# Kernel optimization log

Hardware: AMD Instinct MI355X
Metric: run time of the kernel (lower is better)

Reference implementation:

```python
import jax, jax.numpy as jnp
import numpy as np

B, N, CIN, H, E = 1, 20000, 128, 128, 320000


def setup_inputs() -> dict:
    key = jax.random.key(0)
    ks = jax.random.split(key, 16)
    x = jax.random.normal(ks[0], (B, N, CIN), jnp.float32)
    edge_index = jax.random.randint(ks[1], (2, E), 0, N, dtype=jnp.int64)
    edge_weight = jax.random.uniform(ks[2], (E,), jnp.float32)
    h = jax.random.normal(ks[3], (B, N, H), jnp.float32)
    c = jax.random.normal(ks[4], (B, N, H), jnp.float32)
    # GCN stack params, gate order [i, f, c, o]; 2 layers each (K=2)
    Wx0 = jax.random.normal(ks[5], (4, CIN, H), jnp.float32) / np.float32(np.sqrt(CIN))
    bx0 = jnp.zeros((4, H), jnp.float32)
    Wx1 = jax.random.normal(ks[6], (4, H, H), jnp.float32) / np.float32(np.sqrt(H))
    bx1 = jnp.zeros((4, H), jnp.float32)
    Wh0 = jax.random.normal(ks[7], (4, H, H), jnp.float32) / np.float32(np.sqrt(H))
    bh0 = jnp.zeros((4, H), jnp.float32)
    Wh1 = jax.random.normal(ks[8], (4, H, H), jnp.float32) / np.float32(np.sqrt(H))
    bh1 = jnp.zeros((4, H), jnp.float32)
    wc = jax.random.normal(ks[9], (3, H), jnp.float32) * 0.1  # peephole [i, f, o]
    bg = jnp.zeros((4, H), jnp.float32)  # gate biases [i, f, c, o]
    return dict(x=x, edge_index=edge_index, edge_weight=edge_weight, h=h, c=c,
                Wx0=Wx0, bx0=bx0, Wx1=Wx1, bx1=bx1,
                Wh0=Wh0, bh0=bh0, Wh1=Wh1, bh1=bh1, wc=wc, bg=bg)


def reference(x, edge_index, edge_weight, h, c,
              Wx0, bx0, Wx1, bx1, Wh0, bh0, Wh1, bh1, wc, bg):
    n = x.shape[1]
    src, dst = edge_index[0], edge_index[1]
    loop = jnp.arange(n)
    src2 = jnp.concatenate([src, loop])
    dst2 = jnp.concatenate([dst, loop])
    w2 = jnp.concatenate([edge_weight, jnp.ones((n,), edge_weight.dtype)])
    deg = jax.ops.segment_sum(w2, dst2, num_segments=n)
    dis = jnp.where(deg > 0, jax.lax.rsqrt(jnp.maximum(deg, 1e-12)), 0.0)
    norm = dis[src2] * w2 * dis[dst2]  # sym GCN norm with self loops

    def prop(t):  # t: [..., N, F] -> D^-1/2 (A+I) D^-1/2 t
        lead = t.shape[:-2]
        tf = t.reshape((-1,) + t.shape[-2:])
        m = tf[:, src2, :] * norm[None, :, None]
        agg = jax.vmap(lambda mm: jax.ops.segment_sum(mm, dst2, num_segments=n))(m)
        return agg.reshape(lead + agg.shape[-2:])

    def gcn4(t, W0, b0, W1, b1):  # 2-layer GCN, 4 gates at once
        a = prop(t)  # shared first aggregation: [B,N,F]
        h0 = jax.nn.relu(jnp.einsum('bnc,gch->gbnh', a, W0) + b0[:, None, None, :])
        a1 = prop(h0)  # [4,B,N,H]
        return jnp.einsum('gbnh,ghk->gbnk', a1, W1) + b1[:, None, None, :]

    G = gcn4(x, Wx0, bx0, Wx1, bx1) + gcn4(h, Wh0, bh0, Wh1, bh1)  # [4,B,N,H]
    I = jax.nn.sigmoid(G[0] + wc[0] * c + bg[0])
    F = jax.nn.sigmoid(G[1] + wc[1] * c + bg[1])
    T = jnp.tanh(G[2] + bg[2])
    Cn = F * c + I * T
    O = jax.nn.sigmoid(G[3] + wc[2] * Cn + bg[3])
    Hn = O * jnp.tanh(Cn)
    return (Hn, Cn)
```

## Files before the change

kernel.cpp:

```cpp
#include <hip/hip_runtime.h>
#include <hip/hip_bf16.h>
#include <stdint.h>

#define NN    20000
#define NP    20096
#define EE    320000
#define CH    128
#define GC    512
#define NHtot 2560000

typedef short bf16x8 __attribute__((ext_vector_type(8)));
typedef float f32x4  __attribute__((ext_vector_type(4)));

__device__ __forceinline__ unsigned short f2bf(float f) {
    __hip_bfloat16 b = __float2bfloat16(f);
    union { __hip_bfloat16 b; unsigned short u; } c; c.b = b; return c.u;
}
__device__ __forceinline__ void fma4(uint2 u, float n, float* acc) {
    union { unsigned int i; float f; } t;
    t.i = u.x << 16;         acc[0] += n * t.f;
    t.i = u.x & 0xffff0000u; acc[1] += n * t.f;
    t.i = u.y << 16;         acc[2] += n * t.f;
    t.i = u.y & 0xffff0000u; acc[3] += n * t.f;
}
__device__ __forceinline__ void tof4(uint2 u, float* f) {
    union { unsigned int i; float f; } t;
    t.i = u.x << 16;         f[0] = t.f;
    t.i = u.x & 0xffff0000u; f[1] = t.f;
    t.i = u.y << 16;         f[2] = t.f;
    t.i = u.y & 0xffff0000u; f[3] = t.f;
}
__device__ __forceinline__ uint2 pack4(const float* f) {
    uint2 v;
    v.x = (unsigned int)f2bf(f[0]) | ((unsigned int)f2bf(f[1]) << 16);
    v.y = (unsigned int)f2bf(f[2]) | ((unsigned int)f2bf(f[3]) << 16);
    return v;
}

__global__ void k_cntprep(const int* __restrict__ ei, int* __restrict__ cnt,
                          const float* __restrict__ W0, const float* __restrict__ W1,
                          const float* __restrict__ W2, const float* __restrict__ W3,
                          unsigned short* __restrict__ T0, unsigned short* __restrict__ T1,
                          unsigned short* __restrict__ T2, unsigned short* __restrict__ T3,
                          const float* __restrict__ bx1, const float* __restrict__ bh1,
                          const float* __restrict__ bg, float* __restrict__ btot) {
    int bid = blockIdx.x;
    if (bid < EE / 256) {
        int e = bid * 256 + threadIdx.x;
        atomicAdd(&cnt[ei[EE + e]], 1);
        return;
    }
    int pid = bid - EE / 256;
    int z = pid >> 8, y = (pid >> 6) & 3, xb = pid & 63;
    if (z == 0 && y == 0 && xb < 2) {
        int f = xb * 256 + threadIdx.x;
        btot[f] = bx1[f] + bh1[f] + bg[f];
    }
    const float* W; unsigned short* T;
    switch (z) {
        case 0:  W = W0; T = T0; break;
        case 1:  W = W1; T = T1; break;
        case 2:  W = W2; T = T2; break;
        default: W = W3; T = T3; break;
    }
    int n = xb * 2 + (threadIdx.x >> 7);
    int k = threadIdx.x & 127;
    T[((size_t)y * 128 + n) * 128 + k] = f2bf(W[((size_t)y * 128 + k) * 128 + n]);
}

__global__ void k_scan1(const int* __restrict__ cnt, int* __restrict__ rowoff,
                        int* __restrict__ bsum) {
    __shared__ int wsum[4];
    int i = blockIdx.x * 256 + threadIdx.x;
    int self = (i < NN) ? cnt[i] : 0;
    int lane = threadIdx.x & 63, wid = threadIdx.x >> 6;
    int v = self;
    #pragma unroll
    for (int off = 1; off < 64; off <<= 1) {
        int u = __shfl_up(v, off);
        if (lane >= off) v += u;
    }
    if (lane == 63) wsum[wid] = v;
    __syncthreads();
    int wof = 0;
    for (int k = 0; k < wid; ++k) wof += wsum[k];
    if (i < NN) rowoff[i] = wof + v - self;
    if (threadIdx.x == 255) bsum[blockIdx.x] = wof + v;
}

__global__ void k_scan2(int* __restrict__ bsum) {
    int lane = threadIdx.x;
    int base = 0;
    for (int start = 0; start < 80; start += 64) {
        int i = start + lane;
        int self = (i < 80) ? bsum[i] : 0;
        int v = self;
        #pragma unroll
        for (int off = 1; off < 64; off <<= 1) {
            int u = __shfl_up(v, off);
            if (lane >= off) v += u;
        }
        if (i < 80) bsum[i] = base + v - self;
        base += __shfl(v, 63);
    }
}

__global__ void k_scan3(int* __restrict__ rowoff, const int* __restrict__ bsum,
                        int* __restrict__ cur) {
    int i = blockIdx.x * 256 + threadIdx.x;
    if (i < NN) {
        int v = rowoff[i] + bsum[i >> 8];
        rowoff[i] = v; cur[i] = v;
    }
    if (i == NN) rowoff[NN] = EE;
}

__global__ void k_scatter(const int* __restrict__ ei, const float* __restrict__ ew,
                          int* __restrict__ cur,
                          int* __restrict__ csrs, float* __restrict__ csrw) {
    int e = blockIdx.x * 256 + threadIdx.x;
    if (e >= EE) return;
    int s = ei[e], d = ei[EE + e];
    int p = atomicAdd(&cur[d], 1);
    csrs[p] = s; csrw[p] = ew[e];
}

__global__ __launch_bounds__(256) void k_degcast(
        const float* __restrict__ x, const float* __restrict__ h,
        const int* __restrict__ rowoff, const float* __restrict__ csrw,
        float* __restrict__ dis, unsigned short* __restrict__ xhb) {
    int wid = threadIdx.x >> 6, lane = threadIdx.x & 63;
    int w = blockIdx.x * 4 + wid;
    int e0 = rowoff[w], e1 = rowoff[w + 1];
    float s = 0.f;
    for (int e = e0 + lane; e < e1; e += 64) s += csrw[e];
    #pragma unroll
    for (int off = 32; off; off >>= 1) s += __shfl_xor(s, off);
    float dn = rsqrtf(fmaxf(1.0f + s, 1e-12f));
    if (lane == 0) dis[w] = dn;
    const float* src = (lane < 32) ? x + (size_t)w * CH + lane * 4
                                   : h + (size_t)w * CH + (lane - 32) * 4;
    float4 v = *(const float4*)src;
    float f[4] = { dn * v.x, dn * v.y, dn * v.z, dn * v.w };
    *(uint2*)(xhb + (size_t)w * 256 + lane * 4) = pack4(f);
}

__global__ __launch_bounds__(128) void k_prop256(
        const unsigned short* __restrict__ tab, unsigned short* __restrict__ o,
        const int* __restrict__ rowoff, const int* __restrict__ csrs,
        const float* __restrict__ csrw, const float* __restrict__ dis) {
    int w = blockIdx.x * 2 + (threadIdx.x >> 6);
    int lane = threadIdx.x & 63;
    const uint2* T2 = (const uint2*)tab;
    float acc[4];
    tof4(T2[(size_t)w * 64 + lane], acc);
    int e = rowoff[w], e1 = rowoff[w + 1];
    for (; e + 4 <= e1; e += 4) {
        int   s0 = csrs[e],   s1 = csrs[e+1], s2 = csrs[e+2], s3 = csrs[e+3];
        float n0 = csrw[e],   n1 = csrw[e+1], n2 = csrw[e+2], n3 = csrw[e+3];
        uint2 u0 = T2[(size_t)s0 * 64 + lane];
        uint2 u1 = T2[(size_t)s1 * 64 + lane];
        uint2 u2 = T2[(size_t)s2 * 64 + lane];
        uint2 u3 = T2[(size_t)s3 * 64 + lane];
        fma4(u0, n0, acc); fma4(u1, n1, acc); fma4(u2, n2, acc); fma4(u3, n3, acc);
    }
    for (; e < e1; ++e) {
        fma4(T2[(size_t)csrs[e] * 64 + lane], csrw[e], acc);
    }
    float dw = dis[w];
    #pragma unroll
    for (int j = 0; j < 4; ++j) acc[j] *= dw;
    ((uint2*)o)[(size_t)w * 64 + lane] = pack4(acc);
}

#define SWZ(r, c8) (((r) << 4) + ((c8) ^ ((r) & 15)))

__global__ __launch_bounds__(256) void k_gemm1(
        const unsigned short* __restrict__ A,
        const unsigned short* __restrict__ Wtx, const unsigned short* __restrict__ Wth,
        const float* __restrict__ bx0, const float* __restrict__ bh0,
        unsigned short* __restrict__ outx, unsigned short* __restrict__ outh) {
    __shared__ uint4 As[2048];
    __shared__ uint4 Bs[2048];
    const int side = blockIdx.z;
    const int aoff = side * 128;
    const unsigned short* Wt = side ? Wth : Wtx;
    const float* bias        = side ? bh0 : bx0;
    unsigned short* out      = side ? outh : outx;

    const int    g    = blockIdx.y;
    const size_t row0 = (size_t)blockIdx.x * 128;
    const int    t    = threadIdx.x;

    #pragma unroll
    for (int p = 0; p < 8; ++p) {
        int id = t + 256 * p, r = id >> 4, c8 = id & 15;
        As[SWZ(r, c8)] = *(const uint4*)(A + (row0 + r) * 256 + aoff + c8 * 8);
    }
    const unsigned short* Wg = Wt + (size_t)g * 16384;
    #pragma unroll
    for (int p = 0; p < 8; ++p) {
        int id = t + 256 * p, r = id >> 4, c8 = id & 15;
        Bs[SWZ(r, c8)] = *(const uint4*)(Wg + r * CH + c8 * 8);
    }
    __syncthreads();

    const int wid = t >> 6, l = t & 63;
    const int m0 = (wid >> 1) * 64, n0 = (wid & 1) * 64;
    const int lm = l & 15, q = l >> 4;
    f32x4 acc[4][4];
    #pragma unroll
    for (int i = 0; i < 4; ++i)
        #pragma unroll
        for (int j = 0; j < 4; ++j) { acc[i][j][0]=0.f; acc[i][j][1]=0.f; acc[i][j][2]=0.f; acc[i][j][3]=0.f; }

    #pragma unroll
    for (int kc = 0; kc < 4; ++kc) {
        int c8 = kc * 4 + q;
        bf16x8 a[4], b[4];
        #pragma unroll
        for (int i = 0; i < 4; ++i) { int r = m0 + i * 16 + lm; a[i] = *(const bf16x8*)&As[SWZ(r, c8)]; }
        #pragma unroll
        for (int j = 0; j < 4; ++j) { int r = n0 + j * 16 + lm; b[j] = *(const bf16x8*)&Bs[SWZ(r, c8)]; }
        #pragma unroll
        for (int i = 0; i < 4; ++i)
            #pragma unroll
            for (int j = 0; j < 4; ++j)
                acc[i][j] = __builtin_amdgcn_mfma_f32_16x16x32_bf16(a[i], b[j], acc[i][j], 0, 0, 0);
    }

    #pragma unroll
    for (int j = 0; j < 4; ++j) {
        float bb = bias[g * CH + n0 + j * 16 + lm];
        #pragma unroll
        for (int i = 0; i < 4; ++i)
            #pragma unroll
            for (int r = 0; r < 4; ++r) {
                int rowl = m0 + i * 16 + q * 4 + r;
                int col  = n0 + j * 16 + lm;
                out[(row0 + rowl) * GC + g * CH + col] = f2bf(fmaxf(acc[i][j][r] + bb, 0.f));
            }
    }
}

__global__ __launch_bounds__(256) void k_gemm2(
        const unsigned short* __restrict__ A1, const unsigned short* __restrict__ A2,
        const unsigned short* __restrict__ Wt1, const unsigned short* __restrict__ Wt2,
        const float* __restrict__ dis, unsigned short* __restrict__ outS) {
    __shared__ uint4 As[2048];
    __shared__ uint4 Bs[2048];
    const int    g    = blockIdx.y;
    const size_t row0 = (size_t)blockIdx.x * 128;
    const int    t    = threadIdx.x;
    const int wid = t >> 6, l = t & 63;
    const int m0 = (wid >> 1) * 64, n0 = (wid & 1) * 64;
    const int lm = l & 15, q = l >> 4;
    f32x4 acc[4][4];
    #pragma unroll
    for (int i = 0; i < 4; ++i)
        #pragma unroll
        for (int j = 0; j < 4; ++j) { acc[i][j][0]=0.f; acc[i][j][1]=0.f; acc[i][j][2]=0.f; acc[i][j][3]=0.f; }

    for (int side = 0; side < 2; ++side) {
        if (side) __syncthreads();
        const unsigned short* Ap = side ? A2 : A1;
        const unsigned short* Wg = (side ? Wt2 : Wt1) + (size_t)g * 16384;
        #pragma unroll
        for (int p = 0; p < 8; ++p) {
            int id = t + 256 * p, r = id >> 4, c8 = id & 15;
            As[SWZ(r, c8)] = *(const uint4*)(Ap + (row0 + r) * GC + g * CH + c8 * 8);
        }
        #pragma unroll
        for (int p = 0; p < 8; ++p) {
            int id = t + 256 * p, r = id >> 4, c8 = id & 15;
            Bs[SWZ(r, c8)] = *(const uint4*)(Wg + r * CH + c8 * 8);
        }
        __syncthreads();
        #pragma unroll
        for (int kc = 0; kc < 4; ++kc) {
            int c8 = kc * 4 + q;
            bf16x8 a[4], b[4];
            #pragma unroll
            for (int i = 0; i < 4; ++i) { int r = m0 + i * 16 + lm; a[i] = *(const bf16x8*)&As[SWZ(r, c8)]; }
            #pragma unroll
            for (int j = 0; j < 4; ++j) { int r = n0 + j * 16 + lm; b[j] = *(const bf16x8*)&Bs[SWZ(r, c8)]; }
            #pragma unroll
            for (int i = 0; i < 4; ++i)
                #pragma unroll
                for (int j = 0; j < 4; ++j)
                    acc[i][j] = __builtin_amdgcn_mfma_f32_16x16x32_bf16(a[i], b[j], acc[i][j], 0, 0, 0);
        }
    }

    #pragma unroll
    for (int j = 0; j < 4; ++j)
        #pragma unroll
        for (int i = 0; i < 4; ++i)
            #pragma unroll
            for (int r = 0; r < 4; ++r) {
                int rowl = m0 + i * 16 + q * 4 + r;
                int col  = n0 + j * 16 + lm;
                float dr = dis[row0 + rowl];
                outS[(row0 + rowl) * GC + g * CH + col] = f2bf(dr * acc[i][j][r]);
            }
}

#define GIDX(f) ((f) + ((f) >> 5))
__global__ __launch_bounds__(128) void k_prop512g(
        const unsigned short* __restrict__ Sb, float* __restrict__ out,
        const int* __restrict__ rowoff, const int* __restrict__ csrs,
        const float* __restrict__ csrw, const float* __restrict__ dis,
        const float* __restrict__ c, const float* __restrict__ btot,
        const float* __restrict__ wc) {
    __shared__ float gbuf[528];
    int half = threadIdx.x >> 6, lane = threadIdx.x & 63;
    int w = blockIdx.x;
    const uint2* S2 = (const uint2*)Sb;
    size_t foff = (size_t)half * 64 + lane;
    float acc[4];
    tof4(S2[(size_t)w * 128 + foff], acc);
    int e = rowoff[w], e1 = rowoff[w + 1];
    for (; e + 4 <= e1; e += 4) {
        int   s0 = csrs[e],   s1 = csrs[e+1], s2 = csrs[e+2], s3 = csrs[e+3];
        float n0 = csrw[e],   n1 = csrw[e+1], n2 = csrw[e+2], n3 = csrw[e+3];
        uint2 u0 = S2[(size_t)s0 * 128 + foff];
        uint2 u1 = S2[(size_t)s1 * 128 + foff];
        uint2 u2 = S2[(size_t)s2 * 128 + foff];
        uint2 u3 = S2[(size_t)s3 * 128 + foff];
        fma4(u0, n0, acc); fma4(u1, n1, acc); fma4(u2, n2, acc); fma4(u3, n3, acc);
    }
    for (; e < e1; ++e) {
        fma4(S2[(size_t)csrs[e] * 128 + foff], csrw[e], acc);
    }
    float dw = dis[w];
    #pragma unroll
    for (int j = 0; j < 4; ++j) {
        int f = half * 256 + lane * 4 + j;
        gbuf[GIDX(f)] = dw * acc[j];
    }
    __syncthreads();
    int hh = threadIdx.x;
    float g0 = gbuf[GIDX(hh)]       + btot[hh];
    float g1 = gbuf[GIDX(128 + hh)] + btot[128 + hh];
    float g2 = gbuf[GIDX(256 + hh)] + btot[256 + hh];
    float g3 = gbuf[GIDX(384 + hh)] + btot[384 + hh];
    float cv = c[(size_t)w * CH + hh];
    float I  = 1.f / (1.f + expf(-(g0 + wc[hh]       * cv)));
    float F  = 1.f / (1.f + expf(-(g1 + wc[128 + hh] * cv)));
    float T  = tanhf(g2);
    float Cn = F * cv + I * T;
    float O  = 1.f / (1.f + expf(-(g3 + wc[256 + hh] * Cn)));
    out[(size_t)w * CH + hh]         = O * tanhf(Cn);
    out[NHtot + (size_t)w * CH + hh] = Cn;
}

extern "C" void kernel_launch(void* const* d_in, const int* in_sizes, int n_in,
                              void* d_out, int out_size, void* d_ws, size_t ws_size,
                              hipStream_t stream) {
    (void)in_sizes; (void)n_in; (void)out_size; (void)ws_size;
    const float* x   = (const float*)d_in[0];
    const int*   ei  = (const int*)d_in[1];
    const float* ew  = (const float*)d_in[2];
    const float* h   = (const float*)d_in[3];
    const float* c   = (const float*)d_in[4];
    const float* Wx0 = (const float*)d_in[5];
    const float* bx0 = (const float*)d_in[6];
    const float* Wx1 = (const float*)d_in[7];
    const float* bx1 = (const float*)d_in[8];
    const float* Wh0 = (const float*)d_in[9];
    const float* bh0 = (const float*)d_in[10];
    const float* Wh1 = (const float*)d_in[11];
    const float* bh1 = (const float*)d_in[12];
    const float* wc  = (const float*)d_in[13];
    const float* bg  = (const float*)d_in[14];
    float* out = (float*)d_out;

    float* wsf  = (float*)d_ws;
    float* dis  = wsf;
    int*   cnt  = (int*)(wsf + 20480);
    int*   row  = (int*)(wsf + 40960);
    int*   cur  = (int*)(wsf + 61696);
    int*   bsum = (int*)(wsf + 82176);
    float* btot = wsf + 82432;
    int*   csrs = (int*)(wsf + 82944);
    float* csrw = wsf + 402944;
    unsigned short* Wt0x = (unsigned short*)(wsf + 722944);
    unsigned short* Wt0h = (unsigned short*)(wsf + 755712);
    unsigned short* Wt1x = (unsigned short*)(wsf + 788480);
    unsigned short* Wt1h = (unsigned short*)(wsf + 821248);
    unsigned short* xhb  = (unsigned short*)(wsf + 854016);
    unsigned short* axh  = (unsigned short*)(wsf + 3426304);
    unsigned short* h0x  = (unsigned short*)(wsf + 5998592);
    unsigned short* h0h  = (unsigned short*)(wsf + 11143168);
    unsigned short* Sb   = (unsigned short*)(wsf + 16287744);

    hipMemsetAsync(cnt, 0, 20480 * sizeof(int), stream);

    k_cntprep<<<EE / 256 + 1024, 256, 0, stream>>>(ei, cnt,
                                                   Wx0, Wh0, Wx1, Wh1,
                                                   Wt0x, Wt0h, Wt1x, Wt1h,
                                                   bx1, bh1, bg, btot);
    k_scan1  <<<80, 256, 0, stream>>>(cnt, row, bsum);
    k_scan2  <<<1, 64, 0, stream>>>(bsum);
    k_scan3  <<<80, 256, 0, stream>>>(row, bsum, cur);
    k_scatter<<<EE / 256, 256, 0, stream>>>(ei, ew, cur, csrs, csrw);

    k_degcast<<<NN / 4, 256, 0, stream>>>(x, h, row, csrw, dis, xhb);

    k_prop256<<<NN / 2, 128, 0, stream>>>(xhb, axh, row, csrs, csrw, dis);

    dim3 g1(NP / 128, 4, 2);
    k_gemm1<<<g1, 256, 0, stream>>>(axh, Wt0x, Wt0h, bx0, bh0, h0x, h0h);
    dim3 g2(NP / 128, 4);
    k_gemm2<<<g2, 256, 0, stream>>>(h0x, h0h, Wt1x, Wt1h, dis, Sb);

    k_prop512g<<<NN, 128, 0, stream>>>(Sb, out, row, csrs, csrw, dis, c, btot, wc);
}
```

Baseline: 258.1 us.

## Merge scan passes, fuse degree into count atomics, and unroll gather loops

Edge degree sums are now accumulated with float atomics during the count pass instead of a per-node CSR reduction. The three-kernel scan is replaced by a single 1024-thread block scan, and the scatter and degree/cast kernels are merged into one launch. This cuts several launches and serial dependencies. The propagation gather loops gain an 8-wide unrolled body to put more loads in flight. The cost is extra float atomics and nondeterministic degree summation order.

```diff
diff --git a/kernel.cpp b/kernel.cpp
--- a/kernel.cpp
+++ b/kernel.cpp
@@ -37,7 +37,8 @@
     return v;
 }
 
-__global__ void k_cntprep(const int* __restrict__ ei, int* __restrict__ cnt,
+__global__ void k_cntprep(const int* __restrict__ ei, const float* __restrict__ ew,
+                          int* __restrict__ cnt, float* __restrict__ deg,
                           const float* __restrict__ W0, const float* __restrict__ W1,
                           const float* __restrict__ W2, const float* __restrict__ W3,
                           unsigned short* __restrict__ T0, unsigned short* __restrict__ T1,
@@ -47,7 +48,9 @@
     int bid = blockIdx.x;
     if (bid < EE / 256) {
         int e = bid * 256 + threadIdx.x;
-        atomicAdd(&cnt[ei[EE + e]], 1);
+        int d = ei[EE + e];
+        atomicAdd(&cnt[d], 1);
+        atomicAdd(&deg[d], ew[e]);
         return;
     }
     int pid = bid - EE / 256;
@@ -68,75 +71,57 @@
     T[((size_t)y * 128 + n) * 128 + k] = f2bf(W[((size_t)y * 128 + k) * 128 + n]);
 }
 
-__global__ void k_scan1(const int* __restrict__ cnt, int* __restrict__ rowoff,
-                        int* __restrict__ bsum) {
-    __shared__ int wsum[4];
-    int i = blockIdx.x * 256 + threadIdx.x;
-    int self = (i < NN) ? cnt[i] : 0;
-    int lane = threadIdx.x & 63, wid = threadIdx.x >> 6;
-    int v = self;
+__global__ __launch_bounds__(1024) void k_scanA(const int* __restrict__ cnt,
+                                                int* __restrict__ rowoff,
+                                                int* __restrict__ cur) {
+    __shared__ int wtot[16];
+    int t = threadIdx.x;
+    int base = t * 20;
+    int loc[20];
+    int s = 0;
+    #pragma unroll
+    for (int j = 0; j < 20; ++j) {
+        int i = base + j;
+        int v = (i < NN) ? cnt[i] : 0;
+        loc[j] = s; s += v;
+    }
+    int lane = t & 63, wv = t >> 6;
+    int ps = s;
     #pragma unroll
     for (int off = 1; off < 64; off <<= 1) {
-        int u = __shfl_up(v, off);
-        if (lane >= off) v += u;
-    }
-    if (lane == 63) wsum[wid] = v;
+        int u = __shfl_up(ps, off);
+        if (lane >= off) ps += u;
+    }
+    if (lane == 63) wtot[wv] = ps;
     __syncthreads();
     int wof = 0;
-    for (int k = 0; k < wid; ++k) wof += wsum[k];
-    if (i < NN) rowoff[i] = wof + v - self;
-    if (threadIdx.x == 255) bsum[blockIdx.x] = wof + v;
-}
-
-__global__ void k_scan2(int* __restrict__ bsum) {
-    int lane = threadIdx.x;
-    int base = 0;
-    for (int start = 0; start < 80; start += 64) {
-        int i = start + lane;
-        int self = (i < 80) ? bsum[i] : 0;
-        int v = self;
-        #pragma unroll
-        for (int off = 1; off < 64; off <<= 1) {
-            int u = __shfl_up(v, off);
-            if (lane >= off) v += u;
-        }
-        if (i < 80) bsum[i] = base + v - self;
-        base += __shfl(v, 63);
-    }
-}
-
-__global__ void k_scan3(int* __restrict__ rowoff, const int* __restrict__ bsum,
-                        int* __restrict__ cur) {
-    int i = blockIdx.x * 256 + threadIdx.x;
-    if (i < NN) {
-        int v = rowoff[i] + bsum[i >> 8];
-        rowoff[i] = v; cur[i] = v;
-    }
-    if (i == NN) rowoff[NN] = EE;
-}
-
-__global__ void k_scatter(const int* __restrict__ ei, const float* __restrict__ ew,
+    for (int k = 0; k < wv; ++k) wof += wtot[k];
+    int tstart = wof + ps - s;
+    #pragma unroll
+    for (int j = 0; j < 20; ++j) {
+        int i = base + j;
+        if (i < NN) { int v = tstart + loc[j]; rowoff[i] = v; cur[i] = v; }
+    }
+    if (t == 0) rowoff[NN] = EE;
+}
+
+__global__ void k_scatdeg(const int* __restrict__ ei, const float* __restrict__ ew,
                           int* __restrict__ cur,
-                          int* __restrict__ csrs, float* __restrict__ csrw) {
-    int e = blockIdx.x * 256 + threadIdx.x;
-    if (e >= EE) return;
-    int s = ei[e], d = ei[EE + e];
-    int p = atomicAdd(&cur[d], 1);
-    csrs[p] = s; csrw[p] = ew[e];
-}
-
-__global__ __launch_bounds__(256) void k_degcast(
-        const float* __restrict__ x, const float* __restrict__ h,
-        const int* __restrict__ rowoff, const float* __restrict__ csrw,
-        float* __restrict__ dis, unsigned short* __restrict__ xhb) {
+                          int* __restrict__ csrs, float* __restrict__ csrw,
+                          const float* __restrict__ deg,
+                          const float* __restrict__ x, const float* __restrict__ h,
+                          float* __restrict__ dis, unsigned short* __restrict__ xhb) {
+    int bid = blockIdx.x;
+    if (bid < EE / 256) {
+        int e = bid * 256 + threadIdx.x;
+        int s = ei[e], d = ei[EE + e];
+        int p = atomicAdd(&cur[d], 1);
+        csrs[p] = s; csrw[p] = ew[e];
+        return;
+    }
     int wid = threadIdx.x >> 6, lane = threadIdx.x & 63;
-    int w = blockIdx.x * 4 + wid;
-    int e0 = rowoff[w], e1 = rowoff[w + 1];
-    float s = 0.f;
-    for (int e = e0 + lane; e < e1; e += 64) s += csrw[e];
-    #pragma unroll
-    for (int off = 32; off; off >>= 1) s += __shfl_xor(s, off);
-    float dn = rsqrtf(fmaxf(1.0f + s, 1e-12f));
+    int w = (bid - EE / 256) * 4 + wid;
+    float dn = rsqrtf(fmaxf(1.0f + deg[w], 1e-12f));
     if (lane == 0) dis[w] = dn;
     const float* src = (lane < 32) ? x + (size_t)w * CH + lane * 4
                                    : h + (size_t)w * CH + (lane - 32) * 4;
@@ -155,6 +140,22 @@
     float acc[4];
     tof4(T2[(size_t)w * 64 + lane], acc);
     int e = rowoff[w], e1 = rowoff[w + 1];
+    for (; e + 8 <= e1; e += 8) {
+        int   s0 = csrs[e],   s1 = csrs[e+1], s2 = csrs[e+2], s3 = csrs[e+3];
+        int   s4 = csrs[e+4], s5 = csrs[e+5], s6 = csrs[e+6], s7 = csrs[e+7];
+        uint2 u0 = T2[(size_t)s0 * 64 + lane];
+        uint2 u1 = T2[(size_t)s1 * 64 + lane];
+        uint2 u2 = T2[(size_t)s2 * 64 + lane];
+        uint2 u3 = T2[(size_t)s3 * 64 + lane];
+        uint2 u4 = T2[(size_t)s4 * 64 + lane];
+        uint2 u5 = T2[(size_t)s5 * 64 + lane];
+        uint2 u6 = T2[(size_t)s6 * 64 + lane];
+        uint2 u7 = T2[(size_t)s7 * 64 + lane];
+        float n0 = csrw[e],   n1 = csrw[e+1], n2 = csrw[e+2], n3 = csrw[e+3];
+        float n4 = csrw[e+4], n5 = csrw[e+5], n6 = csrw[e+6], n7 = csrw[e+7];
+        fma4(u0, n0, acc); fma4(u1, n1, acc); fma4(u2, n2, acc); fma4(u3, n3, acc);
+        fma4(u4, n4, acc); fma4(u5, n5, acc); fma4(u6, n6, acc); fma4(u7, n7, acc);
+    }
     for (; e + 4 <= e1; e += 4) {
         int   s0 = csrs[e],   s1 = csrs[e+1], s2 = csrs[e+2], s3 = csrs[e+3];
         float n0 = csrw[e],   n1 = csrw[e+1], n2 = csrw[e+2], n3 = csrw[e+3];
@@ -320,6 +321,22 @@
     float acc[4];
     tof4(S2[(size_t)w * 128 + foff], acc);
     int e = rowoff[w], e1 = rowoff[w + 1];
+    for (; e + 8 <= e1; e += 8) {
+        int   s0 = csrs[e],   s1 = csrs[e+1], s2 = csrs[e+2], s3 = csrs[e+3];
+        int   s4 = csrs[e+4], s5 = csrs[e+5], s6 = csrs[e+6], s7 = csrs[e+7];
+        uint2 u0 = S2[(size_t)s0 * 128 + foff];
+        uint2 u1 = S2[(size_t)s1 * 128 + foff];
+        uint2 u2 = S2[(size_t)s2 * 128 + foff];
+        uint2 u3 = S2[(size_t)s3 * 128 + foff];
+        uint2 u4 = S2[(size_t)s4 * 128 + foff];
+        uint2 u5 = S2[(size_t)s5 * 128 + foff];
+        uint2 u6 = S2[(size_t)s6 * 128 + foff];
+        uint2 u7 = S2[(size_t)s7 * 128 + foff];
+        float n0 = csrw[e],   n1 = csrw[e+1], n2 = csrw[e+2], n3 = csrw[e+3];
+        float n4 = csrw[e+4], n5 = csrw[e+5], n6 = csrw[e+6], n7 = csrw[e+7];
+        fma4(u0, n0, acc); fma4(u1, n1, acc); fma4(u2, n2, acc); fma4(u3, n3, acc);
+        fma4(u4, n4, acc); fma4(u5, n5, acc); fma4(u6, n6, acc); fma4(u7, n7, acc);
+    }
     for (; e + 4 <= e1; e += 4) {
         int   s0 = csrs[e],   s1 = csrs[e+1], s2 = csrs[e+2], s3 = csrs[e+3];
         float n0 = csrw[e],   n1 = csrw[e+1], n2 = csrw[e+2], n3 = csrw[e+3];
@@ -378,34 +395,31 @@
     float* wsf  = (float*)d_ws;
     float* dis  = wsf;
     int*   cnt  = (int*)(wsf + 20480);
-    int*   row  = (int*)(wsf + 40960);
-    int*   cur  = (int*)(wsf + 61696);
-    int*   bsum = (int*)(wsf + 82176);
-    float* btot = wsf + 82432;
-    int*   csrs = (int*)(wsf + 82944);
-    float* csrw = wsf + 402944;
-    unsigned short* Wt0x = (unsigned short*)(wsf + 722944);
-    unsigned short* Wt0h = (unsigned short*)(wsf + 755712);
-    unsigned short* Wt1x = (unsigned short*)(wsf + 788480);
-    unsigned short* Wt1h = (unsigned short*)(wsf + 821248);
-    unsigned short* xhb  = (unsigned short*)(wsf + 854016);
-    unsigned short* axh  = (unsigned short*)(wsf + 3426304);
-    unsigned short* h0x  = (unsigned short*)(wsf + 5998592);
-    unsigned short* h0h  = (unsigned short*)(wsf + 11143168);
-    unsigned short* Sb   = (unsigned short*)(wsf + 16287744);
-
-    hipMemsetAsync(cnt, 0, 20480 * sizeof(int), stream);
-
-    k_cntprep<<<EE / 256 + 1024, 256, 0, stream>>>(ei, cnt,
+    float* deg  = wsf + 40960;
+    int*   row  = (int*)(wsf + 61440);
+    int*   cur  = (int*)(wsf + 82176);
+    float* btot = wsf + 102656;
+    int*   csrs = (int*)(wsf + 103168);
+    float* csrw = wsf + 423168;
+    unsigned short* Wt0x = (unsigned short*)(wsf + 743168);
+    unsigned short* Wt0h = (unsigned short*)(wsf + 775936);
+    unsigned short* Wt1x = (unsigned short*)(wsf + 808704);
+    unsigned short* Wt1h = (unsigned short*)(wsf + 841472);
+    unsigned short* xhb  = (unsigned short*)(wsf + 874240);
+    unsigned short* axh  = (unsigned short*)(wsf + 3446528);
+    unsigned short* h0x  = (unsigned short*)(wsf + 6018816);
+    unsigned short* h0h  = (unsigned short*)(wsf + 11163392);
+    unsigned short* Sb   = (unsigned short*)(wsf + 16307968);
+
+    hipMemsetAsync(cnt, 0, 2 * 20480 * sizeof(float), stream);
+
+    k_cntprep<<<EE / 256 + 1024, 256, 0, stream>>>(ei, ew, cnt, deg,
                                                    Wx0, Wh0, Wx1, Wh1,
                                                    Wt0x, Wt0h, Wt1x, Wt1h,
                                                    bx1, bh1, bg, btot);
-    k_scan1  <<<80, 256, 0, stream>>>(cnt, row, bsum);
-    k_scan2  <<<1, 64, 0, stream>>>(bsum);
-    k_scan3  <<<80, 256, 0, stream>>>(row, bsum, cur);
-    k_scatter<<<EE / 256, 256, 0, stream>>>(ei, ew, cur, csrs, csrw);
-
-    k_degcast<<<NN / 4, 256, 0, stream>>>(x, h, row, csrw, dis, xhb);
+    k_scanA  <<<1, 1024, 0, stream>>>(cnt, row, cur);
+    k_scatdeg<<<EE / 256 + NN / 4, 256, 0, stream>>>(ei, ew, cur, csrs, csrw,
+                                                     deg, x, h, dis, xhb);
 
     k_prop256<<<NN / 2, 128, 0, stream>>>(xhb, axh, row, csrs, csrw, dis);
 
```

After: 282.4 us. 1.09x slower.
